# Kernel optimization log

Measured on AMD Instinct MI355X. Metric: run time of the kernel, lower is better.

Reference implementation:

```python
import jax, jax.numpy as jnp
import numpy as np

N_QUBITS = 10
DIM = 1 << N_QUBITS  # 1024

# Constant QFT matrix (PennyLane convention: F[j,k] = w^{jk}/sqrt(N), w = exp(2*pi*i/N),
# wire 0 = most significant bit). Symmetric, so state @ F == F @ state per sample.
_jk = (np.outer(np.arange(DIM), np.arange(DIM)) % DIM).astype(np.float64)
QFT_MAT = jnp.asarray((np.exp(2j * np.pi * _jk / DIM) / np.sqrt(DIM)).astype(np.complex64))


def _apply_1q(state, U, q):
    """Apply 2x2 gate U to wire q (wire 0 = MSB). state: [B, DIM] complex."""
    B = state.shape[0]
    left, right = 1 << q, 1 << (N_QUBITS - 1 - q)
    s = state.reshape(B, left, 2, right)
    s = jnp.einsum('ij,bajc->baic', U, s)
    return s.reshape(B, DIM)


def _apply_cnot(state, c, t):
    """CNOT with control c, target t (wire 0 = MSB)."""
    B = state.shape[0]
    a, b = (c, t) if c < t else (t, c)
    s = state.reshape(B, 1 << a, 2, 1 << (b - a - 1), 2, 1 << (N_QUBITS - 1 - b))
    ctrl_ax, tgt_ax = (2, 4) if c < t else (4, 2)
    s0 = jax.lax.index_in_dim(s, 0, ctrl_ax, keepdims=False)
    s1 = jax.lax.index_in_dim(s, 1, ctrl_ax, keepdims=False)
    ta = tgt_ax - 1 if tgt_ax > ctrl_ax else tgt_ax  # target axis after squeezing ctrl
    s1 = jnp.flip(s1, axis=ta)  # X on target when control == 1
    s = jnp.stack([s0, s1], axis=ctrl_ax)
    return s.reshape(B, DIM)


def _rx(t):
    c = jnp.cos(t / 2).astype(jnp.complex64)
    s = (-1j * jnp.sin(t / 2)).astype(jnp.complex64)
    return jnp.stack([jnp.stack([c, s]), jnp.stack([s, c])])


def _ry(t):
    c = jnp.cos(t / 2).astype(jnp.complex64)
    s = jnp.sin(t / 2).astype(jnp.complex64)
    return jnp.stack([jnp.stack([c, -s]), jnp.stack([s, c])])


def _rz(t):
    e = jnp.exp(-0.5j * t.astype(jnp.complex64))
    z = jnp.zeros((), jnp.complex64)
    return jnp.stack([jnp.stack([e, z]), jnp.stack([z, jnp.conj(e)])])


def _forward(x, weights):
    B = x.shape[0]
    # Pad/truncate is a no-op here (x already [B, DIM]); normalize as in the module.
    nrm = jnp.linalg.norm(x, axis=-1, keepdims=True)
    xn = x / jnp.maximum(nrm, 1e-8)
    state = xn.astype(jnp.complex64)  # AmplitudeEmbedding (already unit-norm)
    for q in range(N_QUBITS):
        state = _apply_1q(state, _rx(weights[q, 0]), q)
    for q in range(N_QUBITS):
        state = _apply_1q(state, _ry(weights[q, 1]), q)
    for q in range(N_QUBITS):
        state = _apply_1q(state, _rz(weights[q, 2]), q)
    for q in range(N_QUBITS):
        state = _apply_cnot(state, q, (q + 1) % N_QUBITS)
    for q in range(N_QUBITS):
        state = _apply_1q(state, _ry(weights[q, 3]), q)
    state = state @ QFT_MAT  # QFT (symmetric matrix)
    ex, ey, ez = [], [], []
    for q in range(N_QUBITS):
        s = state.reshape(B, 1 << q, 2, 1 << (N_QUBITS - 1 - q))
        s0, s1 = s[:, :, 0, :], s[:, :, 1, :]
        cross = jnp.sum(jnp.conj(s0) * s1, axis=(1, 2))
        ex.append(2.0 * jnp.real(cross))                # <X_q>
        ey.append(2.0 * jnp.imag(cross))                # <Y_q>
        ez.append(jnp.sum(jnp.abs(s0) ** 2 - jnp.abs(s1) ** 2, axis=(1, 2)))  # <Z_q>
    return jnp.stack(ex + ey + ez, axis=1).astype(jnp.float32)  # [B, 3*N_QUBITS]


def setup_inputs() -> dict:
    key = jax.random.key(0)
    kx, kw = jax.random.split(key)
    x = jax.random.normal(kx, (8192, 1024), dtype=jnp.float32)
    weights = jax.random.normal(kw, (10, 4), dtype=jnp.float32) * 0.01
    return {"x": x, "weights": weights}


def reference(x, weights):
    return _forward(x, weights)
```

## Files before the change

### kernel.cpp

```cpp
#include <hip/hip_runtime.h>


__device__ __forceinline__ float wred(float v) {
    v += __shfl_xor(v, 1);
    v += __shfl_xor(v, 2);
    v += __shfl_xor(v, 4);
    v += __shfl_xor(v, 8);
    v += __shfl_xor(v, 16);
    v += __shfl_xor(v, 32);
    return v;
}

__device__ __forceinline__ int cnotrev(int k) {
    int m = (int)(__brev((unsigned)k) >> 22);
    #pragma unroll
    for (int q = 9; q >= 0; --q) {
        const int pc = (q == 9) ? 0 : 9 - q;
        const int pt = (q == 9) ? 9 : 8 - q;
        m ^= ((m >> pc) & 1) << pt;
    }
    return m;
}

__global__ __launch_bounds__(256) void fused_kernel(const float* __restrict__ w,
                                                    const float* __restrict__ x,
                                                    float* __restrict__ out)
{
    __shared__ float uu[10][8];
    __shared__ float ryc[10], rys[10];
    __shared__ __align__(16) float scr[4][2048];
    const int tid = threadIdx.x;
    const int wv = tid >> 6, l = tid & 63;
    const int row = blockIdx.x * 4 + wv;
    float* bw = scr[wv];

    if (tid < 10) {
        float t0 = w[tid*4 + 0] * 0.5f, t1 = w[tid*4 + 1] * 0.5f;
        float t2 = w[tid*4 + 2] * 0.5f, t3 = w[tid*4 + 3] * 0.5f;
        float s0, c0, s1, c1, s2, c2, s3, c3;
        __sincosf(t0, &s0, &c0);
        __sincosf(t1, &s1, &c1);
        __sincosf(t2, &s2, &c2);
        __sincosf(t3, &s3, &c3);
        uu[tid][0] =  c2*c1*c0 + s2*s1*s0;
        uu[tid][1] =  c2*s1*s0 - s2*c1*c0;
        uu[tid][2] = -(c2*s1*c0 + s2*c1*s0);
        uu[tid][3] =  s2*s1*c0 - c2*c1*s0;
        uu[tid][4] =  c2*s1*c0 + s2*c1*s0;
        uu[tid][5] =  s2*s1*c0 - c2*c1*s0;
        uu[tid][6] =  c2*c1*c0 + s2*s1*s0;
        uu[tid][7] =  s2*c1*c0 - c2*s1*s0;
        ryc[tid] = c3;
        rys[tid] = s3;
    }
    __syncthreads();

    const float* xr = x + (size_t)row * 1024 + l * 16;
    float4 v0 = ((const float4*)xr)[0];
    float4 v1 = ((const float4*)xr)[1];
    float4 v2 = ((const float4*)xr)[2];
    float4 v3 = ((const float4*)xr)[3];
    float ss = v0.x*v0.x + v0.y*v0.y + v0.z*v0.z + v0.w*v0.w
             + v1.x*v1.x + v1.y*v1.y + v1.z*v1.z + v1.w*v1.w
             + v2.x*v2.x + v2.y*v2.y + v2.z*v2.z + v2.w*v2.w
             + v3.x*v3.x + v3.y*v3.y + v3.z*v3.z + v3.w*v3.w;
    ss = wred(ss);
    const float scale = 0.03125f / fmaxf(sqrtf(ss), 1e-8f);

    float2 c[16];
    c[0]  = make_float2(v0.x*scale, 0.f); c[1]  = make_float2(v0.y*scale, 0.f);
    c[2]  = make_float2(v0.z*scale, 0.f); c[3]  = make_float2(v0.w*scale, 0.f);
    c[4]  = make_float2(v1.x*scale, 0.f); c[5]  = make_float2(v1.y*scale, 0.f);
    c[6]  = make_float2(v1.z*scale, 0.f); c[7]  = make_float2(v1.w*scale, 0.f);
    c[8]  = make_float2(v2.x*scale, 0.f); c[9]  = make_float2(v2.y*scale, 0.f);
    c[10] = make_float2(v2.z*scale, 0.f); c[11] = make_float2(v2.w*scale, 0.f);
    c[12] = make_float2(v3.x*scale, 0.f); c[13] = make_float2(v3.y*scale, 0.f);
    c[14] = make_float2(v3.z*scale, 0.f); c[15] = make_float2(v3.w*scale, 0.f);

    #pragma unroll
    for (int p = 0; p < 4; ++p) {
        const float* U = uu[9 - p];
        const float u00r = U[0], u00i = U[1], u01r = U[2], u01i = U[3];
        const float u10r = U[4], u10i = U[5], u11r = U[6], u11i = U[7];
        const int m = 1 << p;
        #pragma unroll
        for (int i = 0; i < 16; ++i) {
            if (i & m) continue;
            const int j = i | m;
            const float ar = c[i].x, ai = c[i].y, br = c[j].x, bi = c[j].y;
            c[i].x = u00r*ar - u00i*ai + u01r*br - u01i*bi;
            c[i].y = u00r*ai + u00i*ar + u01r*bi + u01i*br;
            c[j].x = u10r*ar - u10i*ai + u11r*br - u11i*bi;
            c[j].y = u10r*ai + u10i*ar + u11r*bi + u11i*br;
        }
    }
    #pragma unroll
    for (int e = 0; e < 6; ++e) {
        const float* U = uu[5 - e];
        const int mybit = (l >> e) & 1;
        const float car = mybit ? U[6] : U[0];
        const float cai = mybit ? U[7] : U[1];
        const float cbr = mybit ? U[4] : U[2];
        const float cbi = mybit ? U[5] : U[3];
        #pragma unroll
        for (int i = 0; i < 16; ++i) {
            const float fr = __shfl_xor(c[i].x, 1 << e);
            const float fi = __shfl_xor(c[i].y, 1 << e);
            const float ar = c[i].x, ai = c[i].y;
            c[i].x = car*ar - cai*ai + cbr*fr - cbi*fi;
            c[i].y = car*ai + cai*ar + cbr*fi + cbi*fr;
        }
    }

    #pragma unroll
    for (int j = 0; j < 8; ++j) {
        const int su = l*8 + (j ^ (l & 7));
        ((float4*)bw)[su] = make_float4(c[2*j].x, c[2*j].y, c[2*j+1].x, c[2*j+1].y);
    }
    const int mb = cnotrev(l << 4);
    #pragma unroll
    for (int i = 0; i < 16; ++i) {
        const int m = mb ^ cnotrev(i);
        const int lm = m >> 4, um = (m >> 1) & 7, lo = m & 1;
        const int su = lm*8 + (um ^ (lm & 7));
        c[i] = ((const float2*)bw)[su*2 + lo];
    }

    #pragma unroll
    for (int p = 0; p < 4; ++p) {
        const float cc = ryc[p], sv = rys[p];
        const int m = 1 << p;
        #pragma unroll
        for (int i = 0; i < 16; ++i) {
            if (i & m) continue;
            const int j = i | m;
            const float ar = c[i].x, ai = c[i].y, br = c[j].x, bi = c[j].y;
            c[i].x = cc*ar - sv*br;  c[i].y = cc*ai - sv*bi;
            c[j].x = sv*ar + cc*br;  c[j].y = sv*ai + cc*bi;
        }
    }
    #pragma unroll
    for (int e = 0; e < 6; ++e) {
        const float cc = ryc[4 + e], sv = rys[4 + e];
        const int mybit = (l >> e) & 1;
        const float sel = mybit ? sv : -sv;
        #pragma unroll
        for (int i = 0; i < 16; ++i) {
            const float fr = __shfl_xor(c[i].x, 1 << e);
            const float fi = __shfl_xor(c[i].y, 1 << e);
            c[i].x = cc*c[i].x + sel*fr;
            c[i].y = cc*c[i].y + sel*fi;
        }
    }

    {
        const float TC8[8] = { 1.f,  0.92387953f,  0.70710678f,  0.38268343f,
                               0.f, -0.38268343f, -0.70710678f, -0.92387953f };
        const float TS8[8] = { 0.f,  0.38268343f,  0.70710678f,  0.92387953f,
                               1.f,  0.92387953f,  0.70710678f,  0.38268343f };
        #pragma unroll
        for (int st = 1; st <= 4; ++st) {
            const int hf = 1 << (st - 1);
            #pragma unroll
            for (int i = 0; i < 16; ++i) {
                if (i & hf) continue;
                const int j = i | hf;
                const int tix = (i & (hf - 1)) << (4 - st);
                const float cwv = TC8[tix], swv = TS8[tix];
                const float tr = cwv*c[j].x - swv*c[j].y;
                const float ti = cwv*c[j].y + swv*c[j].x;
                const float ur = c[i].x, ui = c[i].y;
                c[i].x = ur + tr; c[i].y = ui + ti;
                c[j].x = ur - tr; c[j].y = ui - ti;
            }
        }
    }
    {
        const float WC[6] = { 0.98078528f, 0.99518473f, 0.99879546f,
                              0.99969882f, 0.99992470f, 0.99998118f };
        const float WS[6] = { 0.19509032f, 0.09801714f, 0.04906767f,
                              0.02454123f, 0.01227154f, 0.00613588f };
        #pragma unroll
        for (int e2 = 0; e2 < 6; ++e2) {
            const int st = 5 + e2;
            const float astep = 6.28318530717958647f / (float)(1 << st);
            const int mybit = (l >> e2) & 1;
            const float sel = mybit ? -1.f : 1.f;
            const float cW = WC[e2], sW = WS[e2];
            float cb, sb;
            __sincosf(astep * 16.0f * (float)(l & ((1 << e2) - 1)), &sb, &cb);
            float cw = cb, sw = sb;
            #pragma unroll
            for (int i = 0; i < 16; ++i) {
                const float pr = cw*c[i].x - sw*c[i].y;
                const float pi = cw*c[i].y + sw*c[i].x;
                const float vr = mybit ? pr : c[i].x;
                const float vi = mybit ? pi : c[i].y;
                const float fr = __shfl_xor(vr, 1 << e2);
                const float fi = __shfl_xor(vi, 1 << e2);
                c[i].x = fmaf(sel, vr, fr);
                c[i].y = fmaf(sel, vi, fi);
                const float ncw = cw*cW - sw*sW;
                sw = sw*cW + cw*sW;
                cw = ncw;
            }
        }
    }

    #pragma unroll
    for (int j = 0; j < 8; ++j) {
        const int su = l*8 + (j ^ (l & 7));
        ((float4*)bw)[su] = make_float4(c[2*j].x, c[2*j].y, c[2*j+1].x, c[2*j+1].y);
    }

    float P2s = 0.f;
    #pragma unroll
    for (int i = 0; i < 16; ++i)
        P2s += c[i].x*c[i].x + c[i].y*c[i].y;

    float outv = 0.f;

    #pragma unroll
    for (int p = 0; p < 4; ++p) {
        const int m = 1 << p;
        const int q = 9 - p;
        float rr = 0.f, ii = 0.f, zz = 0.f;
        #pragma unroll
        for (int i = 0; i < 16; ++i) {
            if (i & m) continue;
            const int j = i | m;
            rr += c[i].x*c[j].x + c[i].y*c[j].y;
            ii += c[i].x*c[j].y - c[i].y*c[j].x;
            zz += (c[i].x*c[i].x + c[i].y*c[i].y) - (c[j].x*c[j].x + c[j].y*c[j].y);
        }
        rr = wred(rr);
        ii = wred(ii);
        zz = wred(zz);
        outv = (l == q)      ? 2.f*rr : outv;
        outv = (l == 10 + q) ? 2.f*ii : outv;
        outv = (l == 20 + q) ? zz     : outv;
    }

    #pragma unroll
    for (int e = 0; e < 6; ++e) {
        const int q = 5 - e;
        const int part = l ^ (1 << e);
        const int mybit = (l >> e) & 1;
        const float sgn = mybit ? -1.f : 1.f;
        const int j0 = mybit ? 4 : 0;
        float rr = 0.f, ii = 0.f;
        #pragma unroll
        for (int j = 0; j < 4; ++j) {
            const int su = part*8 + ((j0 + j) ^ (part & 7));
            const float4 f = ((const float4*)bw)[su];
            const float2 a0 = c[2*j],     a1 = c[2*j + 1];
            const float2 b0 = c[2*j + 8], b1 = c[2*j + 9];
            const float m0x = mybit ? b0.x : a0.x;
            const float m0y = mybit ? b0.y : a0.y;
            const float m1x = mybit ? b1.x : a1.x;
            const float m1y = mybit ? b1.y : a1.y;
            rr += m0x*f.x + m0y*f.y;
            ii += m0x*f.y - m0y*f.x;
            rr += m1x*f.z + m1y*f.w;
            ii += m1x*f.w - m1y*f.z;
        }
        const float rr_s = wred(rr);
        const float ii_s = wred(sgn * ii);
        const float zz_s = wred(sgn * P2s);
        outv = (l == q)      ? 2.f*rr_s : outv;
        outv = (l == 10 + q) ? 2.f*ii_s : outv;
        outv = (l == 20 + q) ? zz_s     : outv;
    }

    if (l < 30)
        out[(size_t)row * 30 + l] = outv;
}

extern "C" void kernel_launch(void* const* d_in, const int* in_sizes, int n_in,
                              void* d_out, int out_size, void* d_ws, size_t ws_size,
                              hipStream_t stream) {
    const float* x = (const float*)d_in[0];
    const float* w = (const float*)d_in[1];
    float* out = (float*)d_out;
    (void)d_ws; (void)ws_size;

    fused_kernel<<<2048, 256, 0, stream>>>(w, x, out);
}
```

Before: 154.0 us.

## Split each state row across two wavefronts with LDS exchange for top qubit

Each 1024-amplitude row is now handled by two wavefronts of 8 amplitudes per lane instead of one wavefront of 16. Gates on the most significant qubit, the last QFT stage and the related expectation terms go through shared memory with block barriers, and partial outputs are summed in LDS. The grid doubles to 4096 blocks. The aim is to cut register pressure and raise occupancy and latency hiding, at the cost of extra block-wide synchronisation and LDS traffic.

```diff
diff --git a/kernel.cpp b/kernel.cpp
--- a/kernel.cpp
+++ b/kernel.cpp
@@ -1,5 +1,7 @@
 #include <hip/hip_runtime.h>
 
+
+#define SU(k) (((k) & 512) | (((k) & 511) ^ (((k) >> 3) & 7)))
 
 __device__ __forceinline__ float wred(float v) {
     v += __shfl_xor(v, 1);
@@ -28,11 +30,16 @@
 {
     __shared__ float uu[10][8];
     __shared__ float ryc[10], rys[10];
-    __shared__ __align__(16) float scr[4][2048];
+    __shared__ __align__(16) float2 buf[2][1024];
+    __shared__ float nb[2][2];
+    __shared__ float po[2][2][32];
+
     const int tid = threadIdx.x;
     const int wv = tid >> 6, l = tid & 63;
-    const int row = blockIdx.x * 4 + wv;
-    float* bw = scr[wv];
+    const int rw = wv >> 1, pb = wv & 1;
+    const int row = blockIdx.x * 2 + rw;
+    float2* bw = buf[rw];
+    const int kb = (pb << 9) | (l << 3);
 
     if (tid < 10) {
         float t0 = w[tid*4 + 0] * 0.5f, t1 = w[tid*4 + 1] * 0.5f;
@@ -55,36 +62,30 @@
     }
     __syncthreads();
 
-    const float* xr = x + (size_t)row * 1024 + l * 16;
+    const float* xr = x + (size_t)row * 1024 + kb;
     float4 v0 = ((const float4*)xr)[0];
     float4 v1 = ((const float4*)xr)[1];
-    float4 v2 = ((const float4*)xr)[2];
-    float4 v3 = ((const float4*)xr)[3];
     float ss = v0.x*v0.x + v0.y*v0.y + v0.z*v0.z + v0.w*v0.w
-             + v1.x*v1.x + v1.y*v1.y + v1.z*v1.z + v1.w*v1.w
-             + v2.x*v2.x + v2.y*v2.y + v2.z*v2.z + v2.w*v2.w
-             + v3.x*v3.x + v3.y*v3.y + v3.z*v3.z + v3.w*v3.w;
+             + v1.x*v1.x + v1.y*v1.y + v1.z*v1.z + v1.w*v1.w;
     ss = wred(ss);
-    const float scale = 0.03125f / fmaxf(sqrtf(ss), 1e-8f);
-
-    float2 c[16];
-    c[0]  = make_float2(v0.x*scale, 0.f); c[1]  = make_float2(v0.y*scale, 0.f);
-    c[2]  = make_float2(v0.z*scale, 0.f); c[3]  = make_float2(v0.w*scale, 0.f);
-    c[4]  = make_float2(v1.x*scale, 0.f); c[5]  = make_float2(v1.y*scale, 0.f);
-    c[6]  = make_float2(v1.z*scale, 0.f); c[7]  = make_float2(v1.w*scale, 0.f);
-    c[8]  = make_float2(v2.x*scale, 0.f); c[9]  = make_float2(v2.y*scale, 0.f);
-    c[10] = make_float2(v2.z*scale, 0.f); c[11] = make_float2(v2.w*scale, 0.f);
-    c[12] = make_float2(v3.x*scale, 0.f); c[13] = make_float2(v3.y*scale, 0.f);
-    c[14] = make_float2(v3.z*scale, 0.f); c[15] = make_float2(v3.w*scale, 0.f);
-
-    #pragma unroll
-    for (int p = 0; p < 4; ++p) {
+    if (l == 0) nb[rw][pb] = ss;
+    __syncthreads();
+    const float scale = 0.03125f / fmaxf(sqrtf(nb[rw][0] + nb[rw][1]), 1e-8f);
+
+    float2 c[8];
+    c[0] = make_float2(v0.x*scale, 0.f); c[1] = make_float2(v0.y*scale, 0.f);
+    c[2] = make_float2(v0.z*scale, 0.f); c[3] = make_float2(v0.w*scale, 0.f);
+    c[4] = make_float2(v1.x*scale, 0.f); c[5] = make_float2(v1.y*scale, 0.f);
+    c[6] = make_float2(v1.z*scale, 0.f); c[7] = make_float2(v1.w*scale, 0.f);
+
+    #pragma unroll
+    for (int p = 0; p < 3; ++p) {
         const float* U = uu[9 - p];
         const float u00r = U[0], u00i = U[1], u01r = U[2], u01i = U[3];
         const float u10r = U[4], u10i = U[5], u11r = U[6], u11i = U[7];
         const int m = 1 << p;
         #pragma unroll
-        for (int i = 0; i < 16; ++i) {
+        for (int i = 0; i < 8; ++i) {
             if (i & m) continue;
             const int j = i | m;
             const float ar = c[i].x, ai = c[i].y, br = c[j].x, bi = c[j].y;
@@ -96,14 +97,14 @@
     }
     #pragma unroll
     for (int e = 0; e < 6; ++e) {
-        const float* U = uu[5 - e];
+        const float* U = uu[6 - e];
         const int mybit = (l >> e) & 1;
         const float car = mybit ? U[6] : U[0];
         const float cai = mybit ? U[7] : U[1];
         const float cbr = mybit ? U[4] : U[2];
         const float cbi = mybit ? U[5] : U[3];
         #pragma unroll
-        for (int i = 0; i < 16; ++i) {
+        for (int i = 0; i < 8; ++i) {
             const float fr = __shfl_xor(c[i].x, 1 << e);
             const float fi = __shfl_xor(c[i].y, 1 << e);
             const float ar = c[i].x, ai = c[i].y;
@@ -111,27 +112,39 @@
             c[i].y = car*ai + cai*ar + cbr*fi + cbi*fr;
         }
     }
-
-    #pragma unroll
-    for (int j = 0; j < 8; ++j) {
-        const int su = l*8 + (j ^ (l & 7));
-        ((float4*)bw)[su] = make_float4(c[2*j].x, c[2*j].y, c[2*j+1].x, c[2*j+1].y);
-    }
-    const int mb = cnotrev(l << 4);
-    #pragma unroll
-    for (int i = 0; i < 16; ++i) {
-        const int m = mb ^ cnotrev(i);
-        const int lm = m >> 4, um = (m >> 1) & 7, lo = m & 1;
-        const int su = lm*8 + (um ^ (lm & 7));
-        c[i] = ((const float2*)bw)[su*2 + lo];
-    }
-
-    #pragma unroll
-    for (int p = 0; p < 4; ++p) {
+    {
+        const float* U = uu[0];
+        const float car = pb ? U[6] : U[0];
+        const float cai = pb ? U[7] : U[1];
+        const float cbr = pb ? U[4] : U[2];
+        const float cbi = pb ? U[5] : U[3];
+        #pragma unroll
+        for (int i = 0; i < 8; ++i) bw[SU(kb + i)] = c[i];
+        __syncthreads();
+        #pragma unroll
+        for (int i = 0; i < 8; ++i) {
+            const float2 f = bw[SU((kb ^ 512) + i)];
+            const float ar = c[i].x, ai = c[i].y;
+            c[i].x = car*ar - cai*ai + cbr*f.x - cbi*f.y;
+            c[i].y = car*ai + cai*ar + cbr*f.y + cbi*f.x;
+        }
+    }
+
+    __syncthreads();
+    #pragma unroll
+    for (int i = 0; i < 8; ++i) bw[SU(kb + i)] = c[i];
+    __syncthreads();
+    const int mb = cnotrev(kb);
+    #pragma unroll
+    for (int i = 0; i < 8; ++i)
+        c[i] = bw[SU(mb ^ cnotrev(i))];
+
+    #pragma unroll
+    for (int p = 0; p < 3; ++p) {
         const float cc = ryc[p], sv = rys[p];
         const int m = 1 << p;
         #pragma unroll
-        for (int i = 0; i < 16; ++i) {
+        for (int i = 0; i < 8; ++i) {
             if (i & m) continue;
             const int j = i | m;
             const float ar = c[i].x, ai = c[i].y, br = c[j].x, bi = c[j].y;
@@ -141,32 +154,44 @@
     }
     #pragma unroll
     for (int e = 0; e < 6; ++e) {
-        const float cc = ryc[4 + e], sv = rys[4 + e];
+        const float cc = ryc[3 + e], sv = rys[3 + e];
         const int mybit = (l >> e) & 1;
         const float sel = mybit ? sv : -sv;
         #pragma unroll
-        for (int i = 0; i < 16; ++i) {
+        for (int i = 0; i < 8; ++i) {
             const float fr = __shfl_xor(c[i].x, 1 << e);
             const float fi = __shfl_xor(c[i].y, 1 << e);
             c[i].x = cc*c[i].x + sel*fr;
             c[i].y = cc*c[i].y + sel*fi;
         }
     }
-
-    {
-        const float TC8[8] = { 1.f,  0.92387953f,  0.70710678f,  0.38268343f,
-                               0.f, -0.38268343f, -0.70710678f, -0.92387953f };
-        const float TS8[8] = { 0.f,  0.38268343f,  0.70710678f,  0.92387953f,
-                               1.f,  0.92387953f,  0.70710678f,  0.38268343f };
-        #pragma unroll
-        for (int st = 1; st <= 4; ++st) {
+    {
+        const float cc = ryc[9], sv = rys[9];
+        const float sel = pb ? sv : -sv;
+        __syncthreads();
+        #pragma unroll
+        for (int i = 0; i < 8; ++i) bw[SU(kb + i)] = c[i];
+        __syncthreads();
+        #pragma unroll
+        for (int i = 0; i < 8; ++i) {
+            const float2 f = bw[SU((kb ^ 512) + i)];
+            c[i].x = cc*c[i].x + sel*f.x;
+            c[i].y = cc*c[i].y + sel*f.y;
+        }
+    }
+
+    {
+        const float TC4[4] = { 1.f, 0.70710678f, 0.f, -0.70710678f };
+        const float TS4[4] = { 0.f, 0.70710678f, 1.f,  0.70710678f };
+        #pragma unroll
+        for (int st = 1; st <= 3; ++st) {
             const int hf = 1 << (st - 1);
             #pragma unroll
-            for (int i = 0; i < 16; ++i) {
+            for (int i = 0; i < 8; ++i) {
                 if (i & hf) continue;
                 const int j = i | hf;
-                const int tix = (i & (hf - 1)) << (4 - st);
-                const float cwv = TC8[tix], swv = TS8[tix];
+                const int tix = (i & (hf - 1)) << (3 - st);
+                const float cwv = TC4[tix], swv = TS4[tix];
                 const float tr = cwv*c[j].x - swv*c[j].y;
                 const float ti = cwv*c[j].y + swv*c[j].x;
                 const float ur = c[i].x, ui = c[i].y;
@@ -176,57 +201,85 @@
         }
     }
     {
-        const float WC[6] = { 0.98078528f, 0.99518473f, 0.99879546f,
-                              0.99969882f, 0.99992470f, 0.99998118f };
-        const float WS[6] = { 0.19509032f, 0.09801714f, 0.04906767f,
-                              0.02454123f, 0.01227154f, 0.00613588f };
-        #pragma unroll
-        for (int e2 = 0; e2 < 6; ++e2) {
-            const int st = 5 + e2;
+        const float CT2[6][8] = {
+          {1.f,0.92387953f,0.70710678f,0.38268343f,0.f,-0.38268343f,-0.70710678f,-0.92387953f},
+          {1.f,0.98078528f,0.92387953f,0.83146961f,0.70710678f,0.55557023f,0.38268343f,0.19509032f},
+          {1.f,0.99518473f,0.98078528f,0.95694034f,0.92387953f,0.88192126f,0.83146961f,0.77301045f},
+          {1.f,0.99879546f,0.99518473f,0.98917651f,0.98078528f,0.97003125f,0.95694034f,0.94154407f},
+          {1.f,0.99969882f,0.99879546f,0.99729046f,0.99518473f,0.99247953f,0.98917651f,0.98527764f},
+          {1.f,0.99992470f,0.99969882f,0.99932238f,0.99879546f,0.99811811f,0.99729046f,0.99631261f} };
+        const float ST2[6][8] = {
+          {0.f,0.38268343f,0.70710678f,0.92387953f,1.f,0.92387953f,0.70710678f,0.38268343f},
+          {0.f,0.19509032f,0.38268343f,0.55557023f,0.70710678f,0.83146961f,0.92387953f,0.98078528f},
+          {0.f,0.09801714f,0.19509032f,0.29028468f,0.38268343f,0.47139674f,0.55557023f,0.63439328f},
+          {0.f,0.04906767f,0.09801714f,0.14673047f,0.19509032f,0.24298018f,0.29028468f,0.33688985f},
+          {0.f,0.02454123f,0.04906767f,0.07356456f,0.09801714f,0.12241068f,0.14673047f,0.17096189f},
+          {0.f,0.01227154f,0.02454123f,0.03680722f,0.04906767f,0.06132074f,0.07356456f,0.08579731f} };
+        #pragma unroll
+        for (int e = 0; e < 6; ++e) {
+            const int st = 4 + e;
             const float astep = 6.28318530717958647f / (float)(1 << st);
-            const int mybit = (l >> e2) & 1;
+            const int mybit = (l >> e) & 1;
             const float sel = mybit ? -1.f : 1.f;
-            const float cW = WC[e2], sW = WS[e2];
             float cb, sb;
-            __sincosf(astep * 16.0f * (float)(l & ((1 << e2) - 1)), &sb, &cb);
-            float cw = cb, sw = sb;
+            __sincosf(astep * 8.0f * (float)(l & ((1 << e) - 1)), &sb, &cb);
             #pragma unroll
-            for (int i = 0; i < 16; ++i) {
+            for (int i = 0; i < 8; ++i) {
+                const float cw = cb*CT2[e][i] - sb*ST2[e][i];
+                const float sw = sb*CT2[e][i] + cb*ST2[e][i];
                 const float pr = cw*c[i].x - sw*c[i].y;
                 const float pi = cw*c[i].y + sw*c[i].x;
                 const float vr = mybit ? pr : c[i].x;
                 const float vi = mybit ? pi : c[i].y;
-                const float fr = __shfl_xor(vr, 1 << e2);
-                const float fi = __shfl_xor(vi, 1 << e2);
+                const float fr = __shfl_xor(vr, 1 << e);
+                const float fi = __shfl_xor(vi, 1 << e);
                 c[i].x = fmaf(sel, vr, fr);
                 c[i].y = fmaf(sel, vi, fi);
-                const float ncw = cw*cW - sw*sW;
-                sw = sw*cW + cw*sW;
-                cw = ncw;
             }
         }
     }
-
-    #pragma unroll
-    for (int j = 0; j < 8; ++j) {
-        const int su = l*8 + (j ^ (l & 7));
-        ((float4*)bw)[su] = make_float4(c[2*j].x, c[2*j].y, c[2*j+1].x, c[2*j+1].y);
+    {
+        const float WC[8] = {1.f,0.99998118f,0.99992470f,0.99983058f,
+                             0.99969882f,0.99952942f,0.99932238f,0.99907773f};
+        const float WS[8] = {0.f,0.00613588f,0.01227154f,0.01840673f,
+                             0.02454123f,0.03067480f,0.03680722f,0.04293826f};
+        float cb, sb;
+        __sincosf(6.283185307179586f * (float)(l * 8) * (1.0f/1024.0f), &sb, &cb);
+        const float sel = pb ? -1.f : 1.f;
+        __syncthreads();
+        #pragma unroll
+        for (int i = 0; i < 8; ++i) bw[SU(kb + i)] = c[i];
+        __syncthreads();
+        #pragma unroll
+        for (int i = 0; i < 8; ++i) {
+            const float2 f = bw[SU((kb ^ 512) + i)];
+            const float cw = cb*WC[i] - sb*WS[i];
+            const float sw = sb*WC[i] + cb*WS[i];
+            const float zr = pb ? c[i].x : f.x;
+            const float zi = pb ? c[i].y : f.y;
+            const float wr = cw*zr - sw*zi;
+            const float wi = cw*zi + sw*zr;
+            const float ar = pb ? f.x : c[i].x;
+            const float ai = pb ? f.y : c[i].y;
+            c[i].x = fmaf(sel, wr, ar);
+            c[i].y = fmaf(sel, wi, ai);
+        }
     }
 
     float P2s = 0.f;
     #pragma unroll
-    for (int i = 0; i < 16; ++i)
+    for (int i = 0; i < 8; ++i)
         P2s += c[i].x*c[i].x + c[i].y*c[i].y;
 
     float outv = 0.f;
 
     #pragma unroll
-    for (int p = 0; p < 4; ++p) {
+    for (int p = 0; p < 3; ++p) {
         const int m = 1 << p;
         const int q = 9 - p;
         float rr = 0.f, ii = 0.f, zz = 0.f;
         #pragma unroll
-        for (int i = 0; i < 16; ++i) {
+        for (int i = 0; i < 8; ++i) {
             if (i & m) continue;
             const int j = i | m;
             rr += c[i].x*c[j].x + c[i].y*c[j].y;
@@ -243,37 +296,51 @@
 
     #pragma unroll
     for (int e = 0; e < 6; ++e) {
-        const int q = 5 - e;
-        const int part = l ^ (1 << e);
+        const int q = 6 - e;
         const int mybit = (l >> e) & 1;
         const float sgn = mybit ? -1.f : 1.f;
-        const int j0 = mybit ? 4 : 0;
         float rr = 0.f, ii = 0.f;
         #pragma unroll
-        for (int j = 0; j < 4; ++j) {
-            const int su = part*8 + ((j0 + j) ^ (part & 7));
-            const float4 f = ((const float4*)bw)[su];
-            const float2 a0 = c[2*j],     a1 = c[2*j + 1];
-            const float2 b0 = c[2*j + 8], b1 = c[2*j + 9];
-            const float m0x = mybit ? b0.x : a0.x;
-            const float m0y = mybit ? b0.y : a0.y;
-            const float m1x = mybit ? b1.x : a1.x;
-            const float m1y = mybit ? b1.y : a1.y;
-            rr += m0x*f.x + m0y*f.y;
-            ii += m0x*f.y - m0y*f.x;
-            rr += m1x*f.z + m1y*f.w;
-            ii += m1x*f.w - m1y*f.z;
+        for (int i = 0; i < 8; ++i) {
+            const float fr = __shfl_xor(c[i].x, 1 << e);
+            const float fi = __shfl_xor(c[i].y, 1 << e);
+            rr += c[i].x*fr + c[i].y*fi;
+            ii += c[i].x*fi - c[i].y*fr;
         }
         const float rr_s = wred(rr);
         const float ii_s = wred(sgn * ii);
         const float zz_s = wred(sgn * P2s);
-        outv = (l == q)      ? 2.f*rr_s : outv;
-        outv = (l == 10 + q) ? 2.f*ii_s : outv;
-        outv = (l == 20 + q) ? zz_s     : outv;
-    }
-
-    if (l < 30)
-        out[(size_t)row * 30 + l] = outv;
+        outv = (l == q)      ? rr_s : outv;
+        outv = (l == 10 + q) ? ii_s : outv;
+        outv = (l == 20 + q) ? zz_s : outv;
+    }
+
+    {
+        __syncthreads();
+        #pragma unroll
+        for (int i = 0; i < 8; ++i) bw[SU(kb + i)] = c[i];
+        __syncthreads();
+        float rr = 0.f, ii = 0.f;
+        if (pb == 0) {
+            #pragma unroll
+            for (int i = 0; i < 8; ++i) {
+                const float2 f = bw[SU(512 + (l << 3) + i)];
+                rr += c[i].x*f.x + c[i].y*f.y;
+                ii += c[i].x*f.y - c[i].y*f.x;
+            }
+        }
+        const float rr_s = wred(rr);
+        const float ii_s = wred(ii);
+        const float zz_s = wred(pb ? -P2s : P2s);
+        outv = (l == 0)  ? 2.f*rr_s : outv;
+        outv = (l == 10) ? 2.f*ii_s : outv;
+        outv = (l == 20) ? zz_s     : outv;
+    }
+
+    if (l < 30) po[rw][pb][l] = outv;
+    __syncthreads();
+    if (pb == 0 && l < 30)
+        out[(size_t)row * 30 + l] = po[rw][0][l] + po[rw][1][l];
 }
 
 extern "C" void kernel_launch(void* const* d_in, const int* in_sizes, int n_in,
@@ -284,5 +351,5 @@
     float* out = (float*)d_out;
     (void)d_ws; (void)ws_size;
 
-    fused_kernel<<<2048, 256, 0, stream>>>(w, x, out);
+    fused_kernel<<<4096, 256, 0, stream>>>(w, x, out);
 }
```

New measurement: 200.4 us. 1.3x slower.
